# Performance work log

Hardware: AMD Instinct MI355X
Metric: run time of the kernel (lower is better)

Reference implementation:

```python
import jax, jax.numpy as jnp
import numpy as np

RADIUS = 0.1      # ball-query radius; also max_dist in collision_error
THRESH = 0.001    # collision threshold
NSAMPLE = 4       # neighbors per query point
EPS = 1e-7
LOSS_WEIGHT = 1.0


def _face_normals(verts, faces):
    # verts: (b, n_v, 3), faces: (b, n_f, 3) int -> unit face normals (b, n_f, 3)
    tri = jax.vmap(lambda V, F: V[F])(verts, faces)  # (b, n_f, 3verts, 3xyz)
    e1 = tri[:, :, 1] - tri[:, :, 0]
    e2 = tri[:, :, 2] - tri[:, :, 0]
    fn = jnp.cross(e1, e2)
    return fn / (jnp.linalg.norm(fn, axis=-1, keepdims=True) + EPS)


def _vertex_normals(faces, fn, n_v):
    # sparse v2f bmm equivalent: average incident face normals per vertex
    def scatter(F, N):
        idx = F.reshape(-1)                    # (3*n_f,) face->vertex ids
        vals = jnp.repeat(N, 3, axis=0)        # each face normal to its 3 verts
        s = jnp.zeros((n_v, 3), N.dtype).at[idx].add(vals)
        c = jnp.zeros((n_v, 1), N.dtype).at[idx].add(jnp.float32(1.0))
        return s / (c + EPS)
    return jax.vmap(scatter)(faces, fn)        # (b, n_v, 3)


def _ball_query(new_xyz, xyz, radius, nsample):
    # PointNet++ ball query: first `nsample` points of xyz within radius of each
    # new_xyz point; unfilled slots repeat the first hit (0 if no hits).
    d2 = jnp.sum((new_xyz[:, :, None, :] - xyz[:, None, :, :]) ** 2, axis=-1)  # (b, nq, nv)
    within = d2 < radius * radius
    c = jnp.cumsum(within.astype(jnp.int32), axis=-1)
    n_within = c[..., -1]
    first_idx = jnp.argmax(within, axis=-1)    # 0 when no hits (matches CUDA kernel)
    slots = []
    for j in range(nsample):
        idx_j = jnp.argmax(within & (c == j + 1), axis=-1)
        slots.append(jnp.where(n_within > j, idx_j, first_idx))
    return jnp.stack(slots, axis=-1)           # (b, nq, nsample)


def _collision_loss(pred, h_state, h_faces):
    faces = jnp.swapaxes(h_faces, 1, 2)                 # (b, n_f, 3)
    human_verts = jnp.swapaxes(h_state, 1, 2)[..., :3]  # (b, n_v, 3)
    n_v = human_verts.shape[1]

    fn = _face_normals(human_verts, faces)
    vn = _vertex_normals(faces, fn, n_v)                # (b, n_v, 3)

    idx = _ball_query(pred, human_verts, RADIUS, NSAMPLE)      # (b, nq, K)
    gxyz = jax.vmap(lambda V, I: V[I])(human_verts, idx)       # (b, nq, K, 3)
    gn = jax.vmap(lambda V, I: V[I])(vn, idx)                  # (b, nq, K, 3)

    diff = pred[:, :, None, :] - gxyz
    gn = gn / (jnp.linalg.norm(gn, axis=-1, keepdims=True) + EPS)
    dot = jnp.sum(diff * gn, axis=-1)                   # (b, nq, K)
    valid_dot = (dot - THRESH) * (dot >= -RADIUS)       # max_dist = radius
    mask = valid_dot < 0
    per_pt = jnp.sum(valid_dot * mask / (jnp.sum(mask, axis=-1, keepdims=True) + EPS), axis=-1) ** 2
    avg_mask = per_pt > 0
    loss = jnp.sum(per_pt)                              # reduction='sum', weight=None
    loss = loss / (jnp.sum(avg_mask) + EPS)
    return LOSS_WEIGHT * loss


def setup_inputs() -> dict:
    key = jax.random.key(0)
    k1, k2, k3, k4 = jax.random.split(key, 4)
    bs, n_pred, n_v, n_f, C = 2, 8192, 6890, 13776, 6
    pred = jax.random.uniform(k1, (bs, n_pred, 3), dtype=jnp.float32)
    label = jax.random.uniform(k2, (bs, n_pred, 3), dtype=jnp.float32)
    h_state = jax.random.uniform(k3, (bs, C, n_v), dtype=jnp.float32)
    h_faces = jax.random.randint(k4, (bs, 3, n_f), 0, n_v, dtype=jnp.int32)
    return {"pred": pred, "label": label, "h_state": h_state, "h_faces": h_faces}


def reference(pred, label, h_state, h_faces):
    # label is unused by collision_error (kept for signature fidelity)
    return _collision_loss(pred, h_state, h_faces)
```

## Files before the change

### kernel.cpp

```cpp
#include <hip/hip_runtime.h>
#include <cstdint>
#include <climits>

#define EPSF 1e-7f
#define NCELL 1000
#define RPAD 0.10002f
#define MAXG 6

__device__ __forceinline__ int cell_of(float x, float y, float z) {
    int cx = min(max((int)(x * 10.0f), 0), 9);
    int cy = min(max((int)(y * 10.0f), 0), 9);
    int cz = min(max((int)(z * 10.0f), 0), 9);
    return (cx * 10 + cy) * 10 + cz;
}

__global__ void k1_face_count(const float* __restrict__ hs,
                              const int* __restrict__ hf,
                              float* __restrict__ svec,
                              float* __restrict__ scnt,
                              int* __restrict__ counts,
                              int n_v, int n_f, int bs) {
    int t = blockIdx.x * blockDim.x + threadIdx.x;
    if (t < bs * n_f) {
        int b = t / n_f;
        int f = t - b * n_f;
        const int* fb = hf + (size_t)b * 3 * n_f;
        int i0 = fb[f];
        int i1 = fb[n_f + f];
        int i2 = fb[2 * n_f + f];
        const float* xs = hs + (size_t)b * 6 * n_v;
        const float* ys = xs + n_v;
        const float* zs = xs + 2 * n_v;
        float ax = xs[i0], ay = ys[i0], az = zs[i0];
        float bx = xs[i1], by = ys[i1], bz = zs[i1];
        float cx = xs[i2], cy = ys[i2], cz = zs[i2];
        float e1x = bx - ax, e1y = by - ay, e1z = bz - az;
        float e2x = cx - ax, e2y = cy - ay, e2z = cz - az;
        float fx = e1y * e2z - e1z * e2y;
        float fy = e1z * e2x - e1x * e2z;
        float fz = e1x * e2y - e1y * e2x;
        float nrm = sqrtf(fx * fx + fy * fy + fz * fz) + EPSF;
        fx /= nrm; fy /= nrm; fz /= nrm;
        float* sb = svec + (size_t)b * n_v * 3;
        float* cb = scnt + (size_t)b * n_v;
        int idx3[3] = {i0, i1, i2};
        #pragma unroll
        for (int k = 0; k < 3; ++k) {
            int i = idx3[k];
            atomicAdd(&sb[i * 3 + 0], fx);
            atomicAdd(&sb[i * 3 + 1], fy);
            atomicAdd(&sb[i * 3 + 2], fz);
            atomicAdd(&cb[i], 1.0f);
        }
    }
    if (t < bs * n_v) {
        int b = t / n_v;
        int v = t - b * n_v;
        const float* xs = hs + (size_t)b * 6 * n_v;
        float x = xs[v], y = xs[n_v + v], z = xs[2 * n_v + v];
        atomicAdd(&counts[b * NCELL + cell_of(x, y, z)], 1);
    }
}

__global__ void k2_build(const float* __restrict__ hs,
                         const float* __restrict__ svec,
                         const float* __restrict__ scnt,
                         const int* __restrict__ counts,
                         int* __restrict__ cellstart,
                         float4* __restrict__ vert,
                         float4* __restrict__ spk,
                         int n_v, int bs, int nvb) {
    __shared__ int cursor_l[NCELL];
    if (blockIdx.x < (unsigned)nvb) {
        int t = blockIdx.x * blockDim.x + threadIdx.x;
        if (t >= bs * n_v) return;
        int b = t / n_v;
        int v = t - b * n_v;
        float cc = scnt[t] + EPSF;
        float vx = svec[t * 3 + 0] / cc;
        float vy = svec[t * 3 + 1] / cc;
        float vz = svec[t * 3 + 2] / cc;
        float nrm = sqrtf(vx * vx + vy * vy + vz * vz) + EPSF;
        const float* xs = hs + (size_t)b * 6 * n_v;
        float x = xs[v], y = xs[n_v + v], z = xs[2 * n_v + v];
        vert[2 * (size_t)t + 0] = make_float4(x, y, z, 0.0f);
        vert[2 * (size_t)t + 1] = make_float4(vx / nrm, vy / nrm, vz / nrm, 0.0f);
        return;
    }
    int batch = blockIdx.x - nvb;
    if (threadIdx.x < 64) {
        int lane = threadIdx.x;
        int local[16];
        int mysum = 0;
        #pragma unroll
        for (int k = 0; k < 16; ++k) {
            int c = lane * 16 + k;
            int v = (c < NCELL) ? counts[batch * NCELL + c] : 0;
            local[k] = v;
            mysum += v;
        }
        int s = mysum;
        #pragma unroll
        for (int off = 1; off < 64; off <<= 1) {
            int n = __shfl_up(s, off);
            if (lane >= off) s += n;
        }
        int excl = s - mysum;
        #pragma unroll
        for (int k = 0; k < 16; ++k) {
            int c = lane * 16 + k;
            if (c < NCELL) {
                cellstart[batch * (NCELL + 1) + c] = excl;
                cursor_l[c] = excl;
                excl += local[k];
            }
        }
        if (lane == 63) cellstart[batch * (NCELL + 1) + NCELL] = s;
    }
    __syncthreads();
    const float* xs = hs + (size_t)batch * 6 * n_v;
    for (int v = threadIdx.x; v < n_v; v += blockDim.x) {
        float x = xs[v], y = xs[n_v + v], z = xs[2 * n_v + v];
        int cell = cell_of(x, y, z);
        int pos = atomicAdd(&cursor_l[cell], 1);
        spk[(size_t)batch * n_v + pos] = make_float4(x, y, z, __int_as_float(v));
    }
}

__global__ void k3_query(const float* __restrict__ pred,
                         const float4* __restrict__ vert,
                         const float4* __restrict__ spk,
                         const int* __restrict__ cellstart,
                         double* __restrict__ partial,
                         float* __restrict__ pcnt,
                         int n_v, int n_pred, int bs) {
    const int lane = threadIdx.x & 63;
    const int wave = threadIdx.x >> 6;
    const int wid = blockIdx.x * 4 + wave;
    const int nq = bs * n_pred;

    float per_pt = 0.0f;
    float is_pos = 0.0f;

    if (wid < nq) {
        const int b = wid / n_pred;
        const float4* vb = vert + 2 * (size_t)b * n_v;
        const float4* sp = spk + (size_t)b * n_v;
        const int* csb = cellstart + b * (NCELL + 1);
        const float px = pred[(size_t)wid * 3 + 0];
        const float py = pred[(size_t)wid * 3 + 1];
        const float pz = pred[(size_t)wid * 3 + 2];

        int xlo = max(0, (int)floorf((px - RPAD) * 10.0f));
        int xhi = min(9, (int)floorf((px + RPAD) * 10.0f));
        int ylo = max(0, (int)floorf((py - RPAD) * 10.0f));
        int yhi = min(9, (int)floorf((py + RPAD) * 10.0f));
        int zlo = max(0, (int)floorf((pz - RPAD) * 10.0f));
        int zhi = min(9, (int)floorf((pz + RPAD) * 10.0f));

        int rs[9], re[9];
        #pragma unroll
        for (int i = 0; i < 9; ++i) {
            int cx = xlo + i / 3;
            int cy = ylo + i % 3;
            bool valid = (cx <= xhi) && (cy <= yhi);
            int rowbase = (min(cx, 9) * 10 + min(cy, 9)) * 10;
            int lo = csb[rowbase + zlo];
            int hi = csb[rowbase + zhi + 1];
            rs[i] = valid ? lo : 0;
            re[i] = valid ? hi : 0;
        }
        int B[10];
        B[0] = 0;
        #pragma unroll
        for (int i = 0; i < 9; ++i) B[i + 1] = B[i] + (re[i] - rs[i]);
        const int T = B[9];
        int D[9];
        #pragma unroll
        for (int i = 0; i < 9; ++i) D[i] = rs[i] - B[i];

        int l0 = INT_MAX, l1 = INT_MAX, l2 = INT_MAX, l3 = INT_MAX;

        if (T > 0) {
            float4 cbuf[MAXG];
            #pragma unroll
            for (int g = 0; g < MAXG; ++g) {
                if (g * 64 < T) {
                    int pc = min(g * 64 + lane, T - 1);
                    int addr = pc + D[0];
                    #pragma unroll
                    for (int i = 1; i < 9; ++i)
                        addr = (pc >= B[i]) ? pc + D[i] : addr;
                    cbuf[g] = sp[addr];
                }
            }
            #pragma unroll
            for (int g = 0; g < MAXG; ++g) {
                if (g * 64 < T) {
                    int p = g * 64 + lane;
                    if (p < T) {
                        float4 c4 = cbuf[g];
                        float dx = px - c4.x;
                        float dy = py - c4.y;
                        float dz = pz - c4.z;
                        float d2 = dx * dx + dy * dy + dz * dz;
                        if (d2 < 0.01f) {
                            int vid = __float_as_int(c4.w);
                            if (vid < l3) {
                                if (vid < l1) {
                                    if (vid < l0) { l3 = l2; l2 = l1; l1 = l0; l0 = vid; }
                                    else          { l3 = l2; l2 = l1; l1 = vid; }
                                } else {
                                    if (vid < l2) { l3 = l2; l2 = vid; }
                                    else          { l3 = vid; }
                                }
                            }
                        }
                    }
                }
            }
            for (int p = MAXG * 64 + lane; p < T; p += 64) {
                int addr = p + D[0];
                #pragma unroll
                for (int i = 1; i < 9; ++i)
                    addr = (p >= B[i]) ? p + D[i] : addr;
                float4 c4 = sp[addr];
                float dx = px - c4.x;
                float dy = py - c4.y;
                float dz = pz - c4.z;
                float d2 = dx * dx + dy * dy + dz * dz;
                if (d2 < 0.01f) {
                    int vid = __float_as_int(c4.w);
                    if (vid < l3) {
                        if (vid < l1) {
                            if (vid < l0) { l3 = l2; l2 = l1; l1 = l0; l0 = vid; }
                            else          { l3 = l2; l2 = l1; l1 = vid; }
                        } else {
                            if (vid < l2) { l3 = l2; l2 = vid; }
                            else          { l3 = vid; }
                        }
                    }
                }
            }
        }

        #pragma unroll
        for (int off = 1; off < 64; off <<= 1) {
            int r0 = __shfl_xor(l3, off);
            int r1 = __shfl_xor(l2, off);
            int r2 = __shfl_xor(l1, off);
            int r3 = __shfl_xor(l0, off);
            int m0 = min(l0, r0);
            int m1 = min(l1, r1);
            int m2 = min(l2, r2);
            int m3 = min(l3, r3);
            int t0 = min(m0, m2), t2 = max(m0, m2);
            int t1 = min(m1, m3), t3 = max(m1, m3);
            l0 = min(t0, t1); l1 = max(t0, t1);
            l2 = min(t2, t3); l3 = max(t2, t3);
        }

        int id0 = (l0 == INT_MAX) ? 0 : l0;
        int id1 = (l1 == INT_MAX) ? id0 : l1;
        int id2 = (l2 == INT_MAX) ? id0 : l2;
        int id3 = (l3 == INT_MAX) ? id0 : l3;
        int ids[4] = {id0, id1, id2, id3};

        float vd[4];
        float cm = 0.0f;
        #pragma unroll
        for (int j = 0; j < 4; ++j) {
            int id = ids[j];
            float4 cj = vb[2 * id + 0];
            float4 nj = vb[2 * id + 1];
            float dx = px - cj.x;
            float dy = py - cj.y;
            float dz = pz - cj.z;
            float dot = dx * nj.x + dy * nj.y + dz * nj.z;
            float w = (dot >= -0.1f) ? 1.0f : 0.0f;
            float v = (dot - 0.001f) * w;
            bool msk = v < 0.0f;
            vd[j] = msk ? v : 0.0f;
            cm += msk ? 1.0f : 0.0f;
        }
        float s = ((vd[0] + vd[1]) + vd[2]) + vd[3];
        float a = s / (cm + EPSF);
        per_pt = a * a;
        is_pos = (per_pt > 0.0f) ? 1.0f : 0.0f;
    }

    __shared__ float ls[4];
    __shared__ float lc[4];
    if (lane == 0) { ls[wave] = per_pt; lc[wave] = is_pos; }
    __syncthreads();
    if (threadIdx.x == 0) {
        partial[blockIdx.x] = (double)ls[0] + (double)ls[1] + (double)ls[2] + (double)ls[3];
        pcnt[blockIdx.x] = ((lc[0] + lc[1]) + lc[2]) + lc[3];
    }
}

__global__ void finalize_kernel(const double* __restrict__ partial,
                                const float* __restrict__ pcnt,
                                int n, float* __restrict__ out) {
    double s = 0.0, c = 0.0;
    for (int i = threadIdx.x; i < n; i += blockDim.x) {
        s += partial[i];
        c += (double)pcnt[i];
    }
    #pragma unroll
    for (int off = 32; off > 0; off >>= 1) {
        s += __shfl_down(s, off);
        c += __shfl_down(c, off);
    }
    __shared__ double ws_s[4];
    __shared__ double ws_c[4];
    int wave = threadIdx.x >> 6;
    int lane = threadIdx.x & 63;
    if (lane == 0) { ws_s[wave] = s; ws_c[wave] = c; }
    __syncthreads();
    if (threadIdx.x == 0) {
        double S = ws_s[0] + ws_s[1] + ws_s[2] + ws_s[3];
        double C = ws_c[0] + ws_c[1] + ws_c[2] + ws_c[3];
        out[0] = (float)(S / (C + 1e-7));
    }
}

extern "C" void kernel_launch(void* const* d_in, const int* in_sizes, int n_in,
                              void* d_out, int out_size, void* d_ws, size_t ws_size,
                              hipStream_t stream) {
    const float* pred    = (const float*)d_in[0];
    const float* h_state = (const float*)d_in[2];
    const int*   h_faces = (const int*)d_in[3];
    float* out = (float*)d_out;

    const int bs = 2;
    const int n_pred = in_sizes[0] / (bs * 3);
    const int n_v    = in_sizes[2] / (bs * 6);
    const int n_f    = in_sizes[3] / (bs * 3);
    const int nq = bs * n_pred;
    const int nblk = (nq + 3) / 4;

    size_t o_svec    = 0;
    size_t o_scnt    = o_svec + (size_t)bs * n_v * 3;
    size_t o_counts  = o_scnt + (size_t)bs * n_v;
    size_t o_zeroend = (o_counts + (size_t)bs * NCELL + 3) & ~(size_t)3;
    size_t o_cs      = o_zeroend;
    size_t o_partial = (o_cs + (size_t)bs * (NCELL + 1) + 1) & ~(size_t)1;
    size_t o_pcnt    = o_partial + 2 * (size_t)nblk;
    size_t o_spk     = (o_pcnt + (size_t)nblk + 3) & ~(size_t)3;
    size_t o_vert    = o_spk + (size_t)bs * n_v * 4;

    float* base = (float*)d_ws;
    float*  svec      = base + o_svec;
    float*  scnt      = base + o_scnt;
    int*    counts    = (int*)(base + o_counts);
    int*    cellstart = (int*)(base + o_cs);
    double* partial   = (double*)(base + o_partial);
    float*  pcnt      = base + o_pcnt;
    float4* spk       = (float4*)(base + o_spk);
    float4* vert      = (float4*)(base + o_vert);

    hipMemsetAsync(d_ws, 0, o_zeroend * sizeof(float), stream);

    int t1 = bs * n_f;
    k1_face_count<<<(t1 + 255) / 256, 256, 0, stream>>>(
        h_state, h_faces, svec, scnt, counts, n_v, n_f, bs);

    int nvb = (bs * n_v + 255) / 256;
    k2_build<<<nvb + bs, 256, 0, stream>>>(
        h_state, svec, scnt, counts, cellstart, vert, spk, n_v, bs, nvb);

    k3_query<<<nblk, 256, 0, stream>>>(
        pred, vert, spk, cellstart, partial, pcnt, n_v, n_pred, bs);

    finalize_kernel<<<1, 256, 0, stream>>>(partial, pcnt, nblk, out);
}
```

Measured before the change: 113.6 us.

## Process four queries per wavefront using 16-lane subgroups in ball query

```diff
diff --git a/kernel.cpp b/kernel.cpp
--- a/kernel.cpp
+++ b/kernel.cpp
@@ -5,7 +5,6 @@
 #define EPSF 1e-7f
 #define NCELL 1000
 #define RPAD 0.10002f
-#define MAXG 6
 
 __device__ __forceinline__ int cell_of(float x, float y, float z) {
     int cx = min(max((int)(x * 10.0f), 0), 9);
@@ -136,20 +135,21 @@
                          int n_v, int n_pred, int bs) {
     const int lane = threadIdx.x & 63;
     const int wave = threadIdx.x >> 6;
-    const int wid = blockIdx.x * 4 + wave;
+    const int sub = lane & 15;
+    const int qid = blockIdx.x * 16 + wave * 4 + (lane >> 4);
     const int nq = bs * n_pred;
 
     float per_pt = 0.0f;
     float is_pos = 0.0f;
 
-    if (wid < nq) {
-        const int b = wid / n_pred;
+    if (qid < nq) {
+        const int b = qid / n_pred;
         const float4* vb = vert + 2 * (size_t)b * n_v;
         const float4* sp = spk + (size_t)b * n_v;
         const int* csb = cellstart + b * (NCELL + 1);
-        const float px = pred[(size_t)wid * 3 + 0];
-        const float py = pred[(size_t)wid * 3 + 1];
-        const float pz = pred[(size_t)wid * 3 + 2];
+        const float px = pred[(size_t)qid * 3 + 0];
+        const float py = pred[(size_t)qid * 3 + 1];
+        const float pz = pred[(size_t)qid * 3 + 2];
 
         int xlo = max(0, (int)floorf((px - RPAD) * 10.0f));
         int xhi = min(9, (int)floorf((px + RPAD) * 10.0f));
@@ -158,73 +158,22 @@
         int zlo = max(0, (int)floorf((pz - RPAD) * 10.0f));
         int zhi = min(9, (int)floorf((pz + RPAD) * 10.0f));
 
-        int rs[9], re[9];
+        int ip = min(sub, 8);
+        int cx = xlo + ip / 3;
+        int cy = ylo + ip % 3;
+        bool valid = (cx <= xhi) && (cy <= yhi) && (sub < 9);
+        int rowbase = (min(cx, 9) * 10 + min(cy, 9)) * 10;
+        int rsv = csb[rowbase + zlo];
+        int rev = csb[rowbase + zhi + 1];
+        if (!valid) rev = rsv;
+
+        int l0 = INT_MAX, l1 = INT_MAX, l2 = INT_MAX, l3 = INT_MAX;
         #pragma unroll
         for (int i = 0; i < 9; ++i) {
-            int cx = xlo + i / 3;
-            int cy = ylo + i % 3;
-            bool valid = (cx <= xhi) && (cy <= yhi);
-            int rowbase = (min(cx, 9) * 10 + min(cy, 9)) * 10;
-            int lo = csb[rowbase + zlo];
-            int hi = csb[rowbase + zhi + 1];
-            rs[i] = valid ? lo : 0;
-            re[i] = valid ? hi : 0;
-        }
-        int B[10];
-        B[0] = 0;
-        #pragma unroll
-        for (int i = 0; i < 9; ++i) B[i + 1] = B[i] + (re[i] - rs[i]);
-        const int T = B[9];
-        int D[9];
-        #pragma unroll
-        for (int i = 0; i < 9; ++i) D[i] = rs[i] - B[i];
-
-        int l0 = INT_MAX, l1 = INT_MAX, l2 = INT_MAX, l3 = INT_MAX;
-
-        if (T > 0) {
-            float4 cbuf[MAXG];
-            #pragma unroll
-            for (int g = 0; g < MAXG; ++g) {
-                if (g * 64 < T) {
-                    int pc = min(g * 64 + lane, T - 1);
-                    int addr = pc + D[0];
-                    #pragma unroll
-                    for (int i = 1; i < 9; ++i)
-                        addr = (pc >= B[i]) ? pc + D[i] : addr;
-                    cbuf[g] = sp[addr];
-                }
-            }
-            #pragma unroll
-            for (int g = 0; g < MAXG; ++g) {
-                if (g * 64 < T) {
-                    int p = g * 64 + lane;
-                    if (p < T) {
-                        float4 c4 = cbuf[g];
-                        float dx = px - c4.x;
-                        float dy = py - c4.y;
-                        float dz = pz - c4.z;
-                        float d2 = dx * dx + dy * dy + dz * dz;
-                        if (d2 < 0.01f) {
-                            int vid = __float_as_int(c4.w);
-                            if (vid < l3) {
-                                if (vid < l1) {
-                                    if (vid < l0) { l3 = l2; l2 = l1; l1 = l0; l0 = vid; }
-                                    else          { l3 = l2; l2 = l1; l1 = vid; }
-                                } else {
-                                    if (vid < l2) { l3 = l2; l2 = vid; }
-                                    else          { l3 = vid; }
-                                }
-                            }
-                        }
-                    }
-                }
-            }
-            for (int p = MAXG * 64 + lane; p < T; p += 64) {
-                int addr = p + D[0];
-                #pragma unroll
-                for (int i = 1; i < 9; ++i)
-                    addr = (p >= B[i]) ? p + D[i] : addr;
-                float4 c4 = sp[addr];
+            int rs = __shfl(rsv, i, 16);
+            int re = __shfl(rev, i, 16);
+            for (int p = rs + sub; p < re; p += 16) {
+                float4 c4 = sp[p];
                 float dx = px - c4.x;
                 float dy = py - c4.y;
                 float dz = pz - c4.z;
@@ -245,7 +194,7 @@
         }
 
         #pragma unroll
-        for (int off = 1; off < 64; off <<= 1) {
+        for (int off = 1; off < 16; off <<= 1) {
             int r0 = __shfl_xor(l3, off);
             int r1 = __shfl_xor(l2, off);
             int r2 = __shfl_xor(l1, off);
@@ -289,13 +238,24 @@
         is_pos = (per_pt > 0.0f) ? 1.0f : 0.0f;
     }
 
-    __shared__ float ls[4];
-    __shared__ float lc[4];
-    if (lane == 0) { ls[wave] = per_pt; lc[wave] = is_pos; }
+    __shared__ float ls[16];
+    __shared__ float lc[16];
+    if (sub == 0) {
+        int slot = wave * 4 + (lane >> 4);
+        ls[slot] = per_pt;
+        lc[slot] = is_pos;
+    }
     __syncthreads();
     if (threadIdx.x == 0) {
-        partial[blockIdx.x] = (double)ls[0] + (double)ls[1] + (double)ls[2] + (double)ls[3];
-        pcnt[blockIdx.x] = ((lc[0] + lc[1]) + lc[2]) + lc[3];
+        double ssum = 0.0;
+        float csum = 0.0f;
+        #pragma unroll
+        for (int k = 0; k < 16; ++k) {
+            ssum += (double)ls[k];
+            csum += lc[k];
+        }
+        partial[blockIdx.x] = ssum;
+        pcnt[blockIdx.x] = csum;
     }
 }
 
@@ -338,7 +298,7 @@
     const int n_v    = in_sizes[2] / (bs * 6);
     const int n_f    = in_sizes[3] / (bs * 3);
     const int nq = bs * n_pred;
-    const int nblk = (nq + 3) / 4;
+    const int nblk = (nq + 15) / 16;
 
     size_t o_svec    = 0;
     size_t o_scnt    = o_svec + (size_t)bs * n_v * 3;
```

New measurement: 105.7 us. -6.9%, faster.
